# Optimization experiments

Hardware: AMD Instinct MI355X
Metric: run time of the kernel (lower is better)

Reference implementation:

```python
import jax, jax.numpy as jnp
import numpy as np

B, G, L, S = 4096, 16000, 64, 20000  # batch spots, genes, labels, total spots
LOG_2PI = float(np.log(2.0 * np.pi))


def _log_nb_positive_altparam(x, r, o):
    # NB with total_count r > 0 and logits o (stereoscope parametrization)
    return (jax.lax.lgamma(x + r) - jax.lax.lgamma(r) - jax.lax.lgamma(x + 1.0)
            + x * jax.nn.log_sigmoid(o) + r * jax.nn.log_sigmoid(-o))


def setup_inputs() -> dict:
    key = jax.random.key(0)
    ks = jax.random.split(key, 8)
    x = jax.random.randint(ks[0], (B, G), 0, 100, dtype=jnp.int32)
    y = jax.random.randint(ks[1], (B, 1), 0, L, dtype=jnp.int32)
    ind_x = jax.random.randint(ks[2], (B, 1), 0, S, dtype=jnp.int32)
    W = jax.random.normal(ks[3], (G, L), dtype=jnp.float32)          # fixed dictionary
    px_o = 0.5 * jax.random.normal(ks[4], (G,), dtype=jnp.float32)   # fixed log-odds
    eta = jax.random.normal(ks[5], (G,), dtype=jnp.float32)
    V = jax.random.normal(ks[6], (L + 1, S), dtype=jnp.float32)
    beta = 0.1 * jax.random.normal(ks[7], (G,), dtype=jnp.float32)
    return {"x": x, "y": y, "ind_x": ind_x, "W": W, "px_o": px_o,
            "eta": eta, "V": V, "beta": beta}


def reference(x, y, ind_x, W, px_o, eta, V, beta):
    x_f = x.astype(jnp.float32)                      # [B, G]
    beta_sp = jax.nn.softplus(beta)                  # [G]
    w_sp = jax.nn.softplus(W)                        # [G, L]
    eps_sp = jax.nn.softplus(eta)                    # [G]
    # r_hat = [beta*W | eps]  -> [G, L+1]
    r_hat = jnp.concatenate([beta_sp[:, None] * w_sp, eps_sp[:, None]], axis=1)
    # column-gather from V (embedding lookup over spots), then softplus
    v_ind = jax.nn.softplus(V[:, ind_x[:, 0]])       # [L+1, B]
    # thin matmul, inner dim L+1; px_rate: [B, G]
    px_rate = jnp.einsum("gl,lb->bg", r_hat, v_ind)
    # NB reconstruction loss per spot
    reconst_loss = -jnp.sum(_log_nb_positive_altparam(x_f, px_rate, px_o[None, :]), axis=-1)  # [B]
    # -sum log N(eta; 0, 1)
    neg_log_likelihood_prior = jnp.sum(0.5 * LOG_2PI + 0.5 * eta * eta)
    return (reconst_loss, jnp.float32(0.0), neg_log_likelihood_prior)
```

## Files before the change

kernel.cpp:

```cpp
#include <hip/hip_runtime.h>
#include <hip/hip_bf16.h>
#include <math.h>

#define Gn 16000
#define Bn 4096
#define Ln 64
#define Sn 20000
#define NGT 250
#define NBY 64
#define GSLAB 25

typedef __attribute__((ext_vector_type(8))) short bf16x8;
typedef __attribute__((ext_vector_type(4))) float f32x4;


__device__ __forceinline__ float softplus_precise(float z) {
    return fmaxf(z, 0.0f) + log1pf(__expf(-fabsf(z)));
}

__device__ __forceinline__ float lgamma_pos8(float z) {
    float p = z * (z + 1.f) * (z + 2.f) * (z + 3.f)
                * (z + 4.f) * (z + 5.f) * (z + 6.f) * (z + 7.f);
    float w = z + 8.f;
    return (w - 0.5f) * __logf(w) - w + 0.9189385332046727f
           + __fdividef(1.0f, 12.0f * w) - __logf(p);
}

__device__ __forceinline__ unsigned short f2bf(float f) {
    union { float f; unsigned int u; } v; v.f = f;
    unsigned int r = v.u + 0x7fff + ((v.u >> 16) & 1);
    return (unsigned short)(r >> 16);
}

__device__ __forceinline__ void load_lds16(const void* gsrc, void* lds) {
    __builtin_amdgcn_global_load_lds(
        (const __attribute__((address_space(1))) unsigned int*)gsrc,
        (__attribute__((address_space(3))) unsigned int*)lds,
        16, 0, 0);
}


__global__ void prep_genes(const float* __restrict__ W,
                           const float* __restrict__ px_o,
                           const float* __restrict__ eta,
                           const float* __restrict__ beta,
                           unsigned short* __restrict__ rhB,
                           float4* __restrict__ gcon) {
    int idx = blockIdx.x * 256 + threadIdx.x;
    int g = idx >> 6;
    float bsp = softplus_precise(beta[g]);
    rhB[idx] = f2bf(bsp * softplus_precise(W[idx]));
    if (idx < Gn) {
        float o = px_o[idx];
        float4 c;
        c.x = -softplus_precise(-o) - 1.0f;
        c.y = -softplus_precise(o);
        c.z = softplus_precise(eta[idx]);
        c.w = 0.f;
        gcon[idx] = c;
    }
}

__global__ void prep_spots(const float* __restrict__ V,
                           const int* __restrict__ ind_x,
                           unsigned short* __restrict__ vBg,
                           float* __restrict__ v64) {
    int idx = blockIdx.x * 256 + threadIdx.x;
    int b = idx >> 6, l = idx & 63;
    int s = ind_x[b];
    vBg[idx] = f2bf(softplus_precise(V[l * Sn + s]));
    if (idx < Bn) {
        int s2 = ind_x[idx];
        v64[idx] = softplus_precise(V[Ln * Sn + s2]);
    }
}

__global__ void prior_kernel(const float* __restrict__ eta, float* __restrict__ out) {
    int idx = blockIdx.x * 256 + threadIdx.x;
    float s = 0.f;
    if (idx < Gn) {
        float e = eta[idx];
        s = 0.9189385332046727f + 0.5f * e * e;
    }
    #pragma unroll
    for (int off = 32; off; off >>= 1) s += __shfl_xor(s, off, 64);
    __shared__ float red[4];
    if ((threadIdx.x & 63) == 0) red[threadIdx.x >> 6] = s;
    __syncthreads();
    if (threadIdx.x == 0) atomicAdd(&out[Bn + 1], red[0] + red[1] + red[2] + red[3]);
}


__global__ __launch_bounds__(256) void pack_x(const int* __restrict__ x,
                                              unsigned char* __restrict__ xt) {
    __shared__ unsigned int tile[10 * 1024];
    const int tid = threadIdx.x;
    const int b0 = blockIdx.x * 64;
    const int gs = blockIdx.y;

    #pragma unroll 4
    for (int k = 0; k < 40; ++k) {
        int f = k * 256 + tid;
        int row = f / 160;
        int col4 = f - row * 160;
        int4 v = *(const int4*)&x[(size_t)(b0 + row) * Gn + gs * 640 + col4 * 4];
        unsigned int p = (unsigned int)(v.x & 255)
                       | ((unsigned int)(v.y & 255) << 8)
                       | ((unsigned int)(v.z & 255) << 16)
                       | ((unsigned int)(v.w & 255) << 24);
        int j = col4 >> 4;
        int c = (col4 >> 2) & 3;
        int d = col4 & 3;
        int q = (row >> 2) & 3;
        tile[j * 1024 + row * 16 + ((c ^ q) << 2) + d] = p;
    }
    __syncthreads();

    const int gt0 = gs * 10;
    #pragma unroll
    for (int j = 0; j < 10; ++j) {
        uint4 v = *(const uint4*)&tile[j * 1024 + tid * 4];
        *(uint4*)&xt[((size_t)(gt0 + j) * Bn + b0) * 64 + tid * 16] = v;
    }
}


__global__ __launch_bounds__(256, 6) void main_kernel(
    const unsigned char*  __restrict__ xt,
    const unsigned short* __restrict__ rhB,
    const unsigned short* __restrict__ vBg,
    const float*          __restrict__ v64,
    const float4*         __restrict__ gcon,
    float*                __restrict__ partial) {
    __shared__ __align__(16) unsigned int   sXw[64 * 16];
    __shared__ __align__(16) unsigned short sB[64 * 64];
    __shared__ float lfact[100];
    __shared__ float pred[64];

    const int tid  = threadIdx.x;
    const int wave = tid >> 6, lane = tid & 63;
    const int quad = lane >> 4, ln = lane & 15;
    const int b0 = blockIdx.x * 64;
    const int gt = blockIdx.y;
    const int g0 = gt * 64;

    load_lds16(&xt[((size_t)gt * Bn + b0) * 64 + wave * 1024 + lane * 16],
               (char*)sXw + wave * 1024);
    #pragma unroll
    for (int c = 0; c < 2; ++c) {
        int rowc = wave * 16 + c * 8 + (lane >> 3);
        int slot = (lane & 7) ^ (rowc & 7);
        load_lds16(&rhB[(size_t)(g0 + rowc) * 64 + slot * 8],
                   (char*)sB + (wave * 16 + c * 8) * 128);
    }

    const int mrow = wave * 16 + ln;
    const int xrow = wave * 16 + quad * 4;

    bf16x8 av0 = *(const bf16x8*)&vBg[(b0 + mrow) * 64 + quad * 8];
    bf16x8 av1 = *(const bf16x8*)&vBg[(b0 + mrow) * 64 + 32 + quad * 8];
    float vvr[4];
    #pragma unroll
    for (int r = 0; r < 4; r++) vvr[r] = v64[b0 + xrow + r];
    float4 cc[4];
    #pragma unroll
    for (int nb = 0; nb < 4; nb++) cc[nb] = gcon[g0 + nb * 16 + ln];

    if (tid < 100) lfact[tid] = lgamma_pos8((float)tid + 1.0f);

    __syncthreads();

    f32x4 acc[4];
    #pragma unroll
    for (int nb = 0; nb < 4; nb++) acc[nb] = (f32x4){0.f, 0.f, 0.f, 0.f};
    #pragma unroll
    for (int kb = 0; kb < 2; kb++) {
        bf16x8 af = kb ? av1 : av0;
        #pragma unroll
        for (int nb = 0; nb < 4; nb++) {
            const int nbr = nb * 16 + ln;
            const int boff = nbr * 128 + ((kb * 64 + quad * 16) ^ ((nbr & 7) << 4));
            bf16x8 bfr = *(const bf16x8*)((const char*)sB + boff);
            acc[nb] = __builtin_amdgcn_mfma_f32_16x16x32_bf16(af, bfr, acc[nb], 0, 0, 0);
        }
    }

    const int sh = (ln & 3) * 8;
    float rowacc[4] = {0.f, 0.f, 0.f, 0.f};
    #pragma unroll
    for (int nb = 0; nb < 4; nb++) {
        const float lsp1v = cc[nb].x;
        const float lsnv  = cc[nb].y;
        const float ev    = cc[nb].z;
        #pragma unroll
        for (int r = 0; r < 4; r++) {
            const unsigned int w = sXw[(xrow + r) * 16 + ((nb ^ quad) << 2) + (ln >> 2)];
            const int   xi = (int)((w >> sh) & 255u);
            const float rr = fmaf(ev, vvr[r], acc[nb][r]);
            const float xf = (float)xi;
            const float s  = rr + xf;
            float tt = fmaf(s - 0.5f, __logf(s), -lfact[xi]);
            tt = fmaf(-(rr - 0.5f), __logf(rr), tt);
            tt = fmaf(xf, lsp1v, tt);
            tt = fmaf(rr, lsnv, tt);
            rowacc[r] += tt;
        }
    }

    #pragma unroll
    for (int r = 0; r < 4; r++) {
        float v = rowacc[r];
        v += __shfl_xor(v, 1, 64);
        v += __shfl_xor(v, 2, 64);
        v += __shfl_xor(v, 4, 64);
        v += __shfl_xor(v, 8, 64);
        if (ln == 0) pred[xrow + r] = v;
    }
    __syncthreads();
    if (tid < 64) partial[(size_t)gt * Bn + b0 + tid] = pred[tid];
}

__global__ __launch_bounds__(256) void reduce_kernel(const float* __restrict__ partial,
                                                     float* __restrict__ out) {
    int b = blockIdx.x * 256 + threadIdx.x;
    float s0 = 0.f, s1 = 0.f, s2 = 0.f, s3 = 0.f, s4 = 0.f;
    for (int i = 0; i < NGT; i += 5) {
        s0 += partial[(size_t)(i + 0) * Bn + b];
        s1 += partial[(size_t)(i + 1) * Bn + b];
        s2 += partial[(size_t)(i + 2) * Bn + b];
        s3 += partial[(size_t)(i + 3) * Bn + b];
        s4 += partial[(size_t)(i + 4) * Bn + b];
    }
    out[b] = -(s0 + s1 + s2 + s3 + s4);
}


extern "C" void kernel_launch(void* const* d_in, const int* in_sizes, int n_in,
                              void* d_out, int out_size, void* d_ws, size_t ws_size,
                              hipStream_t stream) {
    const int*   x     = (const int*)d_in[0];
    const int*   ind_x = (const int*)d_in[2];
    const float* W     = (const float*)d_in[3];
    const float* px_o  = (const float*)d_in[4];
    const float* eta   = (const float*)d_in[5];
    const float* V     = (const float*)d_in[6];
    const float* beta  = (const float*)d_in[7];
    float* out = (float*)d_out;

    char* wsb = (char*)d_ws;
    unsigned short* rhB  = (unsigned short*)(wsb);
    unsigned short* vBg  = (unsigned short*)(wsb + 2048000);
    float*          v64  = (float*)(wsb + 2572288);
    float4*         gcon = (float4*)(wsb + 2588672);
    float*          part = (float*)(wsb + 2844672);
    unsigned char*  xt   = (unsigned char*)(wsb + 6940672);

    hipMemsetAsync(d_out, 0, (Bn + 2) * sizeof(float), stream);

    prep_genes<<<(Gn * 64) / 256, 256, 0, stream>>>(W, px_o, eta, beta, rhB, gcon);
    prep_spots<<<(Bn * 64) / 256, 256, 0, stream>>>(V, ind_x, vBg, v64);
    prior_kernel<<<(Gn + 255) / 256, 256, 0, stream>>>(eta, out);

    dim3 pgrid(NBY, GSLAB);
    pack_x<<<pgrid, 256, 0, stream>>>(x, xt);

    dim3 grid(NBY, NGT);
    main_kernel<<<grid, 256, 0, stream>>>(xt, rhB, vBg, v64, gcon, part);

    reduce_kernel<<<Bn / 256, 256, 0, stream>>>(part, out);
}
```

Before: 480.9 us.

## Fuse x byte-packing into main kernel and widen gene tile to 128

Drops the separate pack_x pass, which read int32 x and wrote a transposed byte-packed copy that the main kernel then read back. The main kernel now loads int32 x directly, packs it to bytes in registers and stores it into an XOR-swizzled LDS tile. This removes one kernel launch and a full write and read of the intermediate buffer. The gene tile grows from 64 to 128 with 8 MFMA column blocks, and the grid is reordered so gene tiles vary fastest. In exchange the per-gene constants are now loaded inside the loop, and LDS use and register pressure per block go up.

New measurement: 549.4 us. 14.2% more time.

```diff
diff --git a/kernel.cpp b/kernel.cpp
--- a/kernel.cpp
+++ b/kernel.cpp
@@ -6,9 +6,9 @@
 #define Bn 4096
 #define Ln 64
 #define Sn 20000
-#define NGT 250
+#define GT 128
+#define NGT 125
 #define NBY 64
-#define GSLAB 25
 
 typedef __attribute__((ext_vector_type(8))) short bf16x8;
 typedef __attribute__((ext_vector_type(4))) float f32x4;
@@ -37,6 +37,11 @@
         (const __attribute__((address_space(1))) unsigned int*)gsrc,
         (__attribute__((address_space(3))) unsigned int*)lds,
         16, 0, 0);
+}
+
+__device__ __forceinline__ unsigned int pack4(int4 v) {
+    return (unsigned int)(v.x & 255) | ((unsigned int)(v.y & 255) << 8)
+         | ((unsigned int)(v.z & 255) << 16) | ((unsigned int)(v.w & 255) << 24);
 }
 
 
@@ -91,67 +96,46 @@
 }
 
 
-__global__ __launch_bounds__(256) void pack_x(const int* __restrict__ x,
-                                              unsigned char* __restrict__ xt) {
-    __shared__ unsigned int tile[10 * 1024];
-    const int tid = threadIdx.x;
-    const int b0 = blockIdx.x * 64;
-    const int gs = blockIdx.y;
-
-    #pragma unroll 4
-    for (int k = 0; k < 40; ++k) {
-        int f = k * 256 + tid;
-        int row = f / 160;
-        int col4 = f - row * 160;
-        int4 v = *(const int4*)&x[(size_t)(b0 + row) * Gn + gs * 640 + col4 * 4];
-        unsigned int p = (unsigned int)(v.x & 255)
-                       | ((unsigned int)(v.y & 255) << 8)
-                       | ((unsigned int)(v.z & 255) << 16)
-                       | ((unsigned int)(v.w & 255) << 24);
-        int j = col4 >> 4;
-        int c = (col4 >> 2) & 3;
-        int d = col4 & 3;
-        int q = (row >> 2) & 3;
-        tile[j * 1024 + row * 16 + ((c ^ q) << 2) + d] = p;
-    }
-    __syncthreads();
-
-    const int gt0 = gs * 10;
-    #pragma unroll
-    for (int j = 0; j < 10; ++j) {
-        uint4 v = *(const uint4*)&tile[j * 1024 + tid * 4];
-        *(uint4*)&xt[((size_t)(gt0 + j) * Bn + b0) * 64 + tid * 16] = v;
-    }
-}
-
-
 __global__ __launch_bounds__(256, 6) void main_kernel(
-    const unsigned char*  __restrict__ xt,
+    const int*            __restrict__ x,
     const unsigned short* __restrict__ rhB,
     const unsigned short* __restrict__ vBg,
     const float*          __restrict__ v64,
     const float4*         __restrict__ gcon,
     float*                __restrict__ partial) {
-    __shared__ __align__(16) unsigned int   sXw[64 * 16];
-    __shared__ __align__(16) unsigned short sB[64 * 64];
+    __shared__ __align__(16) unsigned int   sXw[64 * 32];
+    __shared__ __align__(16) unsigned short sB[GT * 64];
     __shared__ float lfact[100];
     __shared__ float pred[64];
 
     const int tid  = threadIdx.x;
     const int wave = tid >> 6, lane = tid & 63;
     const int quad = lane >> 4, ln = lane & 15;
-    const int b0 = blockIdx.x * 64;
-    const int gt = blockIdx.y;
-    const int g0 = gt * 64;
-
-    load_lds16(&xt[((size_t)gt * Bn + b0) * 64 + wave * 1024 + lane * 16],
-               (char*)sXw + wave * 1024);
-    #pragma unroll
-    for (int c = 0; c < 2; ++c) {
-        int rowc = wave * 16 + c * 8 + (lane >> 3);
+    const int gt = blockIdx.x;
+    const int b0 = blockIdx.y * 64;
+    const int g0 = gt * GT;
+
+    #pragma unroll
+    for (int c = 0; c < 4; ++c) {
+        int rowc = wave * 32 + c * 8 + (lane >> 3);
         int slot = (lane & 7) ^ (rowc & 7);
         load_lds16(&rhB[(size_t)(g0 + rowc) * 64 + slot * 8],
-                   (char*)sB + (wave * 16 + c * 8) * 128);
+                   (char*)sB + (wave * 32 + c * 8) * 128);
+    }
+
+    #pragma unroll
+    for (int k = 0; k < 2; ++k) {
+        const int F   = wave * 128 + k * 64 + lane;
+        const int row = F >> 3;
+        const int s   = (F & 7) ^ (row & 7);
+        const int* src = &x[(size_t)(b0 + row) * Gn + g0 + s * 16];
+        int4 a = *(const int4*)(src + 0);
+        int4 b = *(const int4*)(src + 4);
+        int4 c = *(const int4*)(src + 8);
+        int4 d = *(const int4*)(src + 12);
+        uint4 P;
+        P.x = pack4(a); P.y = pack4(b); P.z = pack4(c); P.w = pack4(d);
+        *(uint4*)&sXw[F * 4] = P;
     }
 
     const int mrow = wave * 16 + ln;
@@ -162,22 +146,19 @@
     float vvr[4];
     #pragma unroll
     for (int r = 0; r < 4; r++) vvr[r] = v64[b0 + xrow + r];
-    float4 cc[4];
-    #pragma unroll
-    for (int nb = 0; nb < 4; nb++) cc[nb] = gcon[g0 + nb * 16 + ln];
 
     if (tid < 100) lfact[tid] = lgamma_pos8((float)tid + 1.0f);
 
     __syncthreads();
 
-    f32x4 acc[4];
-    #pragma unroll
-    for (int nb = 0; nb < 4; nb++) acc[nb] = (f32x4){0.f, 0.f, 0.f, 0.f};
+    f32x4 acc[8];
+    #pragma unroll
+    for (int nb = 0; nb < 8; nb++) acc[nb] = (f32x4){0.f, 0.f, 0.f, 0.f};
     #pragma unroll
     for (int kb = 0; kb < 2; kb++) {
         bf16x8 af = kb ? av1 : av0;
         #pragma unroll
-        for (int nb = 0; nb < 4; nb++) {
+        for (int nb = 0; nb < 8; nb++) {
             const int nbr = nb * 16 + ln;
             const int boff = nbr * 128 + ((kb * 64 + quad * 16) ^ ((nbr & 7) << 4));
             bf16x8 bfr = *(const bf16x8*)((const char*)sB + boff);
@@ -188,13 +169,15 @@
     const int sh = (ln & 3) * 8;
     float rowacc[4] = {0.f, 0.f, 0.f, 0.f};
     #pragma unroll
-    for (int nb = 0; nb < 4; nb++) {
-        const float lsp1v = cc[nb].x;
-        const float lsnv  = cc[nb].y;
-        const float ev    = cc[nb].z;
+    for (int nb = 0; nb < 8; nb++) {
+        const float4 cc = gcon[g0 + nb * 16 + ln];
+        const float lsp1v = cc.x;
+        const float lsnv  = cc.y;
+        const float ev    = cc.z;
         #pragma unroll
         for (int r = 0; r < 4; r++) {
-            const unsigned int w = sXw[(xrow + r) * 16 + ((nb ^ quad) << 2) + (ln >> 2)];
+            const int row = xrow + r;
+            const unsigned int w = sXw[row * 32 + ((nb ^ (row & 7)) << 2) + (ln >> 2)];
             const int   xi = (int)((w >> sh) & 255u);
             const float rr = fmaf(ev, vvr[r], acc[nb][r]);
             const float xf = (float)xi;
@@ -253,7 +236,6 @@
     float*          v64  = (float*)(wsb + 2572288);
     float4*         gcon = (float4*)(wsb + 2588672);
     float*          part = (float*)(wsb + 2844672);
-    unsigned char*  xt   = (unsigned char*)(wsb + 6940672);
 
     hipMemsetAsync(d_out, 0, (Bn + 2) * sizeof(float), stream);
 
@@ -261,11 +243,8 @@
     prep_spots<<<(Bn * 64) / 256, 256, 0, stream>>>(V, ind_x, vBg, v64);
     prior_kernel<<<(Gn + 255) / 256, 256, 0, stream>>>(eta, out);
 
-    dim3 pgrid(NBY, GSLAB);
-    pack_x<<<pgrid, 256, 0, stream>>>(x, xt);
-
-    dim3 grid(NBY, NGT);
-    main_kernel<<<grid, 256, 0, stream>>>(xt, rhB, vBg, v64, gcon, part);
+    dim3 grid(NGT, NBY);
+    main_kernel<<<grid, 256, 0, stream>>>(x, rhB, vBg, v64, gcon, part);
 
     reduce_kernel<<<Bn / 256, 256, 0, stream>>>(part, out);
 }
```
